# Kernel tuning notes

Measured on AMD Instinct MI355X. Metric: run time of the kernel, lower is better.

The kernel has to match this reference:

```python
import jax, jax.numpy as jnp
import numpy as np

# ---- config (mirrors cfg in __init__) ----
XB = (-51.2, 51.2, 0.2)
YB = (-51.2, 51.2, 0.2)
ZB = (-10.0, 10.0, 20.0)
C_BEV = 64
BN_EPS = 1e-5

DX = jnp.array([XB[2], YB[2], ZB[2]], jnp.float32)
BX = jnp.array([XB[0] + XB[2] / 2, YB[0] + YB[2] / 2, ZB[0] + ZB[2] / 2], jnp.float32)
NX = (int((XB[1] - XB[0]) / XB[2]), int((YB[1] - YB[0]) / YB[2]), int((ZB[1] - ZB[0]) / ZB[2]))  # (512, 512, 1)


def setup_inputs() -> dict:
    key = jax.random.key(0)
    k1, k2, k3, k4 = jax.random.split(key, 4)
    B, N = 4, 100000
    xy = jax.random.uniform(k1, (B, N, 2), jnp.float32, -54.0, 54.0)   # some points out of bounds
    z = jax.random.uniform(k2, (B, N, 1), jnp.float32, -3.0, 3.0)
    inten = jax.random.uniform(k3, (B, N, 1), jnp.float32)
    points = jnp.concatenate([xy, z, inten], axis=-1)
    W = jax.random.normal(k4, (4, C_BEV), jnp.float32) * 0.5
    b = jnp.zeros((C_BEV,), jnp.float32)
    gamma = jnp.ones((C_BEV,), jnp.float32)
    beta = jnp.zeros((C_BEV,), jnp.float32)
    return {"points": points, "W": W, "b": b, "gamma": gamma, "beta": beta}


def reference(points, W, b, gamma, beta):
    B, N, _ = points.shape
    nx, ny, nz = NX
    p = points.reshape(-1, 4)                      # (B*N, 4)

    # PFN: Linear + BatchNorm1d (training-mode batch stats, biased var) + ReLU
    h = p @ W + b                                  # (B*N, C)
    mu = jnp.mean(h, axis=0)
    var = jnp.var(h, axis=0)
    feat = jax.nn.relu(gamma * (h - mu) * jax.lax.rsqrt(var + BN_EPS) + beta)

    # grid coords: torch .long() truncates toward zero; jnp astype(int) does too
    coords = ((p[:, :3] - (BX - DX / 2.0)) / DX).astype(jnp.int32)
    kept = ((coords[:, 0] >= 0) & (coords[:, 0] < nx)
            & (coords[:, 1] >= 0) & (coords[:, 1] < ny)
            & (coords[:, 2] >= 0) & (coords[:, 2] < nz))

    batch_ix = jnp.repeat(jnp.arange(B, dtype=jnp.int32), N)
    ranks = (batch_ix * (nx * ny * nz)
             + coords[:, 0] + coords[:, 1] * nx + coords[:, 2] * (nx * ny))

    # invalid points -> sentinel bucket (jit-safe replacement for boolean filtering).
    # segment_sum per unique rank == the sort + QuickCumsum trick + scatter-assign.
    flat = B * nx * ny * nz
    ranks = jnp.where(kept, ranks, flat)
    feat = jnp.where(kept[:, None], feat, 0.0)
    bev = jax.ops.segment_sum(feat, ranks, num_segments=flat + 1)[:flat]  # (flat, C)

    bev = bev.reshape(B, nz, ny, nx, C_BEV)
    bev = jnp.transpose(bev, (0, 4, 1, 2, 3)).sum(axis=2)  # (B, C, ny, nx)
    return bev
```

## Files before the change

### kernel.cpp

```cpp
#include <hip/hip_runtime.h>


#define NXG 512
#define NYXG (512 * 512)
#define CB 64
#define SBLK 256
#define GRID_OFF 264192L

__device__ __forceinline__ int coord_mul5(float x, float offx) {
    float t = x - offx;
    asm volatile("" : "+v"(t));
    float q = t * 5.0f;
    asm volatile("" : "+v"(q));
    return (int)q;
}

__global__ void zero_kernel(float4* __restrict__ p, long n4) {
    long i = (long)blockIdx.x * blockDim.x + threadIdx.x;
    long stride = (long)gridDim.x * blockDim.x;
    float4 z = make_float4(0.f, 0.f, 0.f, 0.f);
    for (; i < n4; i += stride) p[i] = z;
}

__global__ void stats_partial(const float4* __restrict__ pts, const float* __restrict__ W,
                              double* __restrict__ S_part, int M) {
    __shared__ float4 tile[256];
    __shared__ double sh1[256], sh2[256];
    int t = threadIdx.x;
    int lane = t & 63;
    int wv = t >> 6;
    float w0 = W[lane], w1 = W[64 + lane], w2 = W[128 + lane], w3 = W[192 + lane];
    double s1 = 0.0, s2 = 0.0;

    int chunk = (M + gridDim.x - 1) / gridDim.x;
    int base = blockIdx.x * chunk;
    int end = base + chunk; if (end > M) end = M;

    for (int i0 = base; i0 < end; i0 += 256) {
        int n = end - i0; if (n > 256) n = 256;
        __syncthreads();
        if (t < n) tile[t] = pts[i0 + t];
        __syncthreads();
        int j0 = wv * 64, j1 = j0 + 64; if (j1 > n) j1 = n;
        for (int j = j0; j < j1; ++j) {
            float4 p = tile[j];
            float q = p.x * w0 + p.y * w1 + p.z * w2 + p.w * w3;
            double qd = (double)q;
            s1 += qd;
            s2 += qd * qd;
        }
    }
    sh1[t] = s1;
    sh2[t] = s2;
    __syncthreads();
    if (t < 64) {
        int c = t;
        S_part[(long)blockIdx.x * 128 + c] =
            (sh1[c] + sh1[64 + c]) + (sh1[128 + c] + sh1[192 + c]);
        S_part[(long)blockIdx.x * 128 + 64 + c] =
            (sh2[c] + sh2[64 + c]) + (sh2[128 + c] + sh2[192 + c]);
    }
}

__global__ void reduce_finalize(const double* __restrict__ S_part,
                                const float* __restrict__ gamma, const float* __restrict__ beta,
                                float* __restrict__ AB, double invM) {
    __shared__ double sh[4][128];
    __shared__ double tot[128];
    int t = threadIdx.x;
    int g = t >> 7, tt = t & 127;
    const double* base = S_part + (long)g * 64 * 128 + tt;
    double a0 = 0.0, a1 = 0.0, a2 = 0.0, a3 = 0.0;
#pragma unroll
    for (int b = 0; b < 64; b += 4) {
        a0 += base[(long)(b + 0) * 128];
        a1 += base[(long)(b + 1) * 128];
        a2 += base[(long)(b + 2) * 128];
        a3 += base[(long)(b + 3) * 128];
    }
    sh[g][tt] = (a0 + a1) + (a2 + a3);
    __syncthreads();
    if (t < 128) tot[t] = (sh[0][t] + sh[1][t]) + (sh[2][t] + sh[3][t]);
    __syncthreads();
    if (t < 64) {
        double mu = tot[t] * invM;
        double var = tot[64 + t] * invM - mu * mu;
        double sc = (double)gamma[t] / sqrt(var + 1e-5);
        AB[t] = (float)sc;
        AB[64 + t] = (float)((double)beta[t] - mu * sc);
    }
}

__global__ void scatter_ws(const float4* __restrict__ pts, const float* __restrict__ W,
                           const float* __restrict__ AB, float* __restrict__ grid,
                           int M, int Nper) {
    int lane = threadIdx.x & 63;
    int wid = blockIdx.x * (blockDim.x >> 6) + (threadIdx.x >> 6);
    int nw = gridDim.x * (blockDim.x >> 6);
    float w0 = W[lane], w1 = W[64 + lane], w2 = W[128 + lane], w3 = W[192 + lane];
    float A = AB[lane], Bc = AB[64 + lane];
    const float offx = -51.1f - 0.1f;
    for (int i = wid; i < M; i += nw) {
        float4 p = pts[i];
        int cx = coord_mul5(p.x, offx);
        int cy = coord_mul5(p.y, offx);
        if (cx < 0 || cx >= NXG || cy < 0 || cy >= NXG) continue;
        int b = i / Nper;
        float q = p.x * w0 + p.y * w1 + p.z * w2 + p.w * w3;
        float f = fmaxf(q * A + Bc, 0.f);
        atomicAdd(&grid[(((long)(b * NXG + cy) * NXG + cx) << 6) + lane], f);
    }
}

__global__ void scatter_direct(const float4* __restrict__ pts, const float* __restrict__ W,
                               const float* __restrict__ AB, float* __restrict__ out,
                               int M, int Nper) {
    int lane = threadIdx.x & 63;
    int wid = blockIdx.x * (blockDim.x >> 6) + (threadIdx.x >> 6);
    int nw = gridDim.x * (blockDim.x >> 6);
    float w0 = W[lane], w1 = W[64 + lane], w2 = W[128 + lane], w3 = W[192 + lane];
    float A = AB[lane], Bc = AB[64 + lane];
    const float offx = -51.1f - 0.1f;
    for (int i = wid; i < M; i += nw) {
        float4 p = pts[i];
        int cx = coord_mul5(p.x, offx);
        int cy = coord_mul5(p.y, offx);
        if (cx < 0 || cx >= NXG || cy < 0 || cy >= NXG) continue;
        int b = i / Nper;
        float q = p.x * w0 + p.y * w1 + p.z * w2 + p.w * w3;
        float f = fmaxf(q * A + Bc, 0.f);
        atomicAdd(&out[((long)(b * CB + lane) * NXG + cy) * NXG + cx], f);
    }
}

__global__ void transpose_kernel(const float* __restrict__ grid, float* __restrict__ out) {
    __shared__ float tile[64][65];
    int blk = blockIdx.x;
    int xt = blk & 7;
    int y = (blk >> 3) & 511;
    int b = blk >> 12;
    int x0 = xt * 64;
    int t = threadIdx.x;

    const float* g = grid + (((long)(b * NXG + y) * NXG + x0) << 6);
    int c = t & 63, i0 = t >> 6;
#pragma unroll
    for (int i = i0; i < 64; i += 4)
        tile[i][c] = g[i * 64 + c];
    __syncthreads();

    int x = t & 63, c0 = t >> 6;
    float* o = out + (long)b * CB * NYXG + y * NXG + x0;
#pragma unroll
    for (int cc = c0; cc < 64; cc += 4)
        o[(long)cc * NYXG + x] = tile[x][cc];
}

extern "C" void kernel_launch(void* const* d_in, const int* in_sizes, int n_in,
                              void* d_out, int out_size, void* d_ws, size_t ws_size,
                              hipStream_t stream) {
    const float4* pts = (const float4*)d_in[0];
    const float* W = (const float*)d_in[1];
    const float* gamma = (const float*)d_in[3];
    const float* beta = (const float*)d_in[4];
    float* out = (float*)d_out;

    int M = in_sizes[0] / 4;
    int B = out_size / (CB * NYXG);
    int Nper = M / B;

    char* wsb = (char*)d_ws;
    float* AB = (float*)(wsb + 1024);
    double* S_part = (double*)(wsb + 2048);
    float* grid = (float*)(wsb + GRID_OFF);

    size_t gridBytes = (size_t)B * NYXG * CB * sizeof(float);
    size_t need = GRID_OFF + gridBytes;

    if (ws_size >= need) {
        zero_kernel<<<2048, 256, 0, stream>>>((float4*)grid, (long)(gridBytes / 16));
        stats_partial<<<SBLK, 256, 0, stream>>>(pts, W, S_part, M);
        reduce_finalize<<<1, 512, 0, stream>>>(S_part, gamma, beta, AB, 1.0 / (double)M);
        scatter_ws<<<2048, 256, 0, stream>>>(pts, W, AB, grid, M, Nper);
        transpose_kernel<<<B * 4096, 256, 0, stream>>>(grid, out);
    } else {
        zero_kernel<<<2048, 256, 0, stream>>>((float4*)out, (long)out_size / 4);
        stats_partial<<<SBLK, 256, 0, stream>>>(pts, W, S_part, M);
        reduce_finalize<<<1, 512, 0, stream>>>(S_part, gamma, beta, AB, 1.0 / (double)M);
        scatter_direct<<<2048, 256, 0, stream>>>(pts, W, AB, out, M, Nper);
    }
}
```

Measured before the change: 252.2 us.

## Replace global grid scatter and transpose with binned counting-sort and LDS accumulation

Drops the large channel-last workspace grid, along with its zeroing, global atomics and transpose pass. Points are instead counted and counting-sorted into bins, one bin per half row of a batch, then each block accumulates its bin in shared memory and writes the channel-major output directly. This removes the 268MB of workspace traffic and the global float atomics. In exchange it adds a serial single-block scan, a reorder pass with atomics, and a 66KB shared accumulator per block that limits occupancy.

```diff
diff --git a/kernel.cpp b/kernel.cpp
--- a/kernel.cpp
+++ b/kernel.cpp
@@ -5,7 +5,6 @@
 #define NYXG (512 * 512)
 #define CB 64
 #define SBLK 256
-#define GRID_OFF 264192L
 
 __device__ __forceinline__ int coord_mul5(float x, float offx) {
     float t = x - offx;
@@ -13,6 +12,11 @@
     float q = t * 5.0f;
     asm volatile("" : "+v"(q));
     return (int)q;
+}
+
+__global__ void zero_ints(int* __restrict__ p, int n) {
+    int i = blockIdx.x * blockDim.x + threadIdx.x;
+    if (i < n) p[i] = 0;
 }
 
 __global__ void zero_kernel(float4* __restrict__ p, long n4) {
@@ -91,24 +95,105 @@
     }
 }
 
-__global__ void scatter_ws(const float4* __restrict__ pts, const float* __restrict__ W,
-                           const float* __restrict__ AB, float* __restrict__ grid,
-                           int M, int Nper) {
-    int lane = threadIdx.x & 63;
-    int wid = blockIdx.x * (blockDim.x >> 6) + (threadIdx.x >> 6);
-    int nw = gridDim.x * (blockDim.x >> 6);
-    float w0 = W[lane], w1 = W[64 + lane], w2 = W[128 + lane], w3 = W[192 + lane];
-    float A = AB[lane], Bc = AB[64 + lane];
-    const float offx = -51.1f - 0.1f;
-    for (int i = wid; i < M; i += nw) {
+__global__ void count_kernel(const float4* __restrict__ pts, int* __restrict__ counts,
+                             int M, int Nper) {
+    int i = blockIdx.x * blockDim.x + threadIdx.x;
+    int stride = gridDim.x * blockDim.x;
+    const float offx = -51.1f - 0.1f;
+    for (; i < M; i += stride) {
         float4 p = pts[i];
         int cx = coord_mul5(p.x, offx);
         int cy = coord_mul5(p.y, offx);
         if (cx < 0 || cx >= NXG || cy < 0 || cy >= NXG) continue;
         int b = i / Nper;
+        int bin = (((b << 9) + cy) << 1) | (cx >> 8);
+        atomicAdd(&counts[bin], 1);
+    }
+}
+
+__global__ void scan_kernel(const int* __restrict__ counts, int* __restrict__ start,
+                            int* __restrict__ cursor, int NB) {
+    __shared__ int partial[256];
+    int t = threadIdx.x;
+    int chunk = (NB + 255) >> 8;
+    int i0 = t * chunk;
+    int i1 = i0 + chunk; if (i1 > NB) i1 = NB; if (i0 > NB) i0 = NB;
+    int s = 0;
+    for (int i = i0; i < i1; ++i) s += counts[i];
+    partial[t] = s;
+    __syncthreads();
+    if (t == 0) {
+        int run = 0;
+        for (int k = 0; k < 256; ++k) { int v = partial[k]; partial[k] = run; run += v; }
+    }
+    __syncthreads();
+    int run = partial[t];
+    for (int i = i0; i < i1; ++i) {
+        int v = counts[i];
+        start[i] = run;
+        cursor[i] = run;
+        run += v;
+    }
+    if (t == 255) start[NB] = run;
+}
+
+__global__ void reorder_kernel(const float4* __restrict__ pts, int* __restrict__ cursor,
+                               float4* __restrict__ pts_s, int M, int Nper) {
+    int i = blockIdx.x * blockDim.x + threadIdx.x;
+    int stride = gridDim.x * blockDim.x;
+    const float offx = -51.1f - 0.1f;
+    for (; i < M; i += stride) {
+        float4 p = pts[i];
+        int cx = coord_mul5(p.x, offx);
+        int cy = coord_mul5(p.y, offx);
+        if (cx < 0 || cx >= NXG || cy < 0 || cy >= NXG) continue;
+        int b = i / Nper;
+        int bin = (((b << 9) + cy) << 1) | (cx >> 8);
+        int idx = atomicAdd(&cursor[bin], 1);
+        pts_s[idx] = p;
+    }
+}
+
+__global__ __launch_bounds__(256) void gather_out(
+    const float4* __restrict__ pts_s, const float* __restrict__ W,
+    const float* __restrict__ AB, const int* __restrict__ bin_start,
+    float* __restrict__ out) {
+    __shared__ float acc[256][65];
+    int t = threadIdx.x;
+    int lane = t & 63, wv = t >> 6;
+    int bin = blockIdx.x;
+    int half = bin & 1;
+    int y = (bin >> 1) & 511;
+    int b = bin >> 10;
+
+    for (int k = t; k < 256 * 65; k += 256) ((float*)acc)[k] = 0.f;
+
+    float w0 = W[lane], w1 = W[64 + lane], w2 = W[128 + lane], w3 = W[192 + lane];
+    float A = AB[lane], Bc = AB[64 + lane];
+    const float offx = -51.1f - 0.1f;
+    int s = bin_start[bin], e = bin_start[bin + 1];
+    __syncthreads();
+
+    int i = s + wv;
+    float4 p = make_float4(0.f, 0.f, 0.f, 0.f);
+    if (i < e) p = pts_s[i];
+    for (; i < e; i += 4) {
+        int in = i + 4;
+        float4 pn = p;
+        if (in < e) pn = pts_s[in];
+        int cx = coord_mul5(p.x, offx);
+        int x = cx - (half << 8);
         float q = p.x * w0 + p.y * w1 + p.z * w2 + p.w * w3;
         float f = fmaxf(q * A + Bc, 0.f);
-        atomicAdd(&grid[(((long)(b * NXG + cy) * NXG + cx) << 6) + lane], f);
+        atomicAdd(&acc[x][lane], f);
+        p = pn;
+    }
+    __syncthreads();
+
+    float* op = out + (size_t)b * CB * NYXG + (size_t)y * NXG + (half << 8) + t;
+#pragma unroll 4
+    for (int j = 0; j < CB; ++j) {
+        op[(size_t)j * NYXG] = acc[t][j];
     }
 }
 
@@ -133,29 +218,6 @@
     }
 }
 
-__global__ void transpose_kernel(const float* __restrict__ grid, float* __restrict__ out) {
-    __shared__ float tile[64][65];
-    int blk = blockIdx.x;
-    int xt = blk & 7;
-    int y = (blk >> 3) & 511;
-    int b = blk >> 12;
-    int x0 = xt * 64;
-    int t = threadIdx.x;
-
-    const float* g = grid + (((long)(b * NXG + y) * NXG + x0) << 6);
-    int c = t & 63, i0 = t >> 6;
-#pragma unroll
-    for (int i = i0; i < 64; i += 4)
-        tile[i][c] = g[i * 64 + c];
-    __syncthreads();
-
-    int x = t & 63, c0 = t >> 6;
-    float* o = out + (long)b * CB * NYXG + y * NXG + x0;
-#pragma unroll
-    for (int cc = c0; cc < 64; cc += 4)
-        o[(long)cc * NYXG + x] = tile[x][cc];
-}
-
 extern "C" void kernel_launch(void* const* d_in, const int* in_sizes, int n_in,
                               void* d_out, int out_size, void* d_ws, size_t ws_size,
                               hipStream_t stream) {
@@ -168,21 +230,28 @@
     int M = in_sizes[0] / 4;
     int B = out_size / (CB * NYXG);
     int Nper = M / B;
+    int NB = B * 1024;
 
     char* wsb = (char*)d_ws;
     float* AB = (float*)(wsb + 1024);
     double* S_part = (double*)(wsb + 2048);
-    float* grid = (float*)(wsb + GRID_OFF);
-
-    size_t gridBytes = (size_t)B * NYXG * CB * sizeof(float);
-    size_t need = GRID_OFF + gridBytes;
+
+    size_t off = 2048 + (size_t)SBLK * 128 * sizeof(double);
+    int* counts = (int*)(wsb + off);     off += (size_t)NB * 4;
+    int* bin_start = (int*)(wsb + off);  off += (size_t)(NB + 1) * 4;
+    int* bin_cursor = (int*)(wsb + off); off += (size_t)NB * 4;
+    off = (off + 15) & ~(size_t)15;
+    float4* pts_s = (float4*)(wsb + off); off += (size_t)M * 16;
+    size_t need = off;
 
     if (ws_size >= need) {
-        zero_kernel<<<2048, 256, 0, stream>>>((float4*)grid, (long)(gridBytes / 16));
+        zero_ints<<<(NB + 255) / 256, 256, 0, stream>>>(counts, NB);
         stats_partial<<<SBLK, 256, 0, stream>>>(pts, W, S_part, M);
+        count_kernel<<<1024, 256, 0, stream>>>(pts, counts, M, Nper);
         reduce_finalize<<<1, 512, 0, stream>>>(S_part, gamma, beta, AB, 1.0 / (double)M);
-        scatter_ws<<<2048, 256, 0, stream>>>(pts, W, AB, grid, M, Nper);
-        transpose_kernel<<<B * 4096, 256, 0, stream>>>(grid, out);
+        scan_kernel<<<1, 256, 0, stream>>>(counts, bin_start, bin_cursor, NB);
+        reorder_kernel<<<1024, 256, 0, stream>>>(pts, bin_cursor, pts_s, M, Nper);
+        gather_out<<<NB, 256, 0, stream>>>(pts_s, W, AB, bin_start, out);
     } else {
         zero_kernel<<<2048, 256, 0, stream>>>((float4*)out, (long)out_size / 4);
         stats_partial<<<SBLK, 256, 0, stream>>>(pts, W, S_part, M);
```

New measurement: 305.8 us. +21.3%, slower.
